# Kernel tuning notes

Hardware: AMD Instinct MI355X
Metric: run time of the kernel (lower is better)

Reference implementation:

```python
import jax, jax.numpy as jnp
import numpy as np
import math

N_NODES = 100000
N_EDGES = 3200000

_SQRT3 = math.sqrt(3.0)
_SQRT5 = math.sqrt(5.0)


def _spherical_harmonics_lmax2(v):
    """e3nn real spherical harmonics, lmax=2, normalize=True, normalization='component'.

    v: [E, 3] edge vectors (not necessarily unit).
    Returns [E, 9] = concat(Y0 [1], Y1 [3], Y2 [5]).
    """
    # normalize=True: evaluate SH on the unit vector
    u = v / jnp.linalg.norm(v, axis=1, keepdims=True)
    x, y, z = u[:, 0], u[:, 1], u[:, 2]
    # l=0 (component norm: *sqrt(1) = 1)
    sh0 = jnp.ones_like(x)
    # l=1 (component norm: *sqrt(3))
    sh1_0 = _SQRT3 * x
    sh1_1 = _SQRT3 * y
    sh1_2 = _SQRT3 * z
    # l=2 raw polynomials (norm-1 at unit vector), then *sqrt(5) for component norm
    x2, y2, z2 = x * x, y * y, z * z
    sh2_0 = _SQRT3 * x * z
    sh2_1 = _SQRT3 * x * y
    sh2_2 = y2 - 0.5 * (x2 + z2)
    sh2_3 = _SQRT3 * y * z
    sh2_4 = 0.5 * _SQRT3 * (z2 - x2)
    sh2 = _SQRT5 * jnp.stack([sh2_0, sh2_1, sh2_2, sh2_3, sh2_4], axis=-1)
    return jnp.concatenate(
        [sh0[:, None], jnp.stack([sh1_0, sh1_1, sh1_2], axis=-1), sh2], axis=-1
    )


def setup_inputs() -> dict:
    key = jax.random.key(0)
    k1, k2, k3 = jax.random.split(key, 3)
    pos = jax.random.normal(k1, (N_NODES, 3), dtype=jnp.float32)
    edge_index = jax.random.randint(k2, (2, N_EDGES), 0, N_NODES, dtype=jnp.int64)
    shift = jax.random.normal(k3, (N_EDGES, 3), dtype=jnp.float32)
    return {"pos": pos, "edge_index": edge_index, "shift": shift}


def reference(pos, edge_index, shift):
    # gather endpoints and form displacement vectors
    edge_vec = pos[edge_index[1]] - pos[edge_index[0]]  # [E, 3]
    edge_vec = edge_vec - shift
    edge_length = jnp.linalg.norm(edge_vec, axis=1)  # [E]
    edge_sh = _spherical_harmonics_lmax2(edge_vec)  # [E, 9]
    return (edge_vec, edge_length, edge_sh)
```

## Files before the change

kernel.cpp:

```cpp
#include <hip/hip_runtime.h>
#include <math.h>


#define SQRT3 1.7320508075688772f
#define SQRT5 2.2360679774997896f

__global__ __launch_bounds__(256) void sh_edge_kernel(
    const float* __restrict__ pos,
    const int*   __restrict__ edge_index,
    const float* __restrict__ shift,
    float* __restrict__ out_vec,
    float* __restrict__ out_len,
    float* __restrict__ out_sh,
    int n_edges)
{
    const int t  = blockIdx.x * blockDim.x + threadIdx.x;
    const int e0 = t * 4;
    if (e0 >= n_edges) return;

    float vx[4], vy[4], vz[4], len[4];
    float ux[4], uy[4], uz[4];

    if (e0 + 3 < n_edges) {
        const int4 src4 = *reinterpret_cast<const int4*>(edge_index + e0);
        const int4 dst4 = *reinterpret_cast<const int4*>(edge_index + n_edges + e0);
        const float4* sb = reinterpret_cast<const float4*>(shift + 3 * (size_t)e0);
        float4 s0 = sb[0], s1 = sb[1], s2 = sb[2];

        const int srcs[4] = {src4.x, src4.y, src4.z, src4.w};
        const int dsts[4] = {dst4.x, dst4.y, dst4.z, dst4.w};
        const float sx[4] = {s0.x, s0.w, s1.z, s2.y};
        const float sy[4] = {s0.y, s1.x, s1.w, s2.z};
        const float sz[4] = {s0.z, s1.y, s2.x, s2.w};

        #pragma unroll
        for (int i = 0; i < 4; ++i) {
            const float* ps = pos + 3 * (size_t)srcs[i];
            const float* pd = pos + 3 * (size_t)dsts[i];
            float x = pd[0] - ps[0] - sx[i];
            float y = pd[1] - ps[1] - sy[i];
            float z = pd[2] - ps[2] - sz[i];
            vx[i] = x; vy[i] = y; vz[i] = z;
            float sq = x * x + y * y + z * z;
            float r  = rsqrtf(sq);
            len[i]   = sq * r;
            ux[i] = x * r; uy[i] = y * r; uz[i] = z * r;
        }

        float4* ov = reinterpret_cast<float4*>(out_vec + 3 * (size_t)e0);
        ov[0] = make_float4(vx[0], vy[0], vz[0], vx[1]);
        ov[1] = make_float4(vy[1], vz[1], vx[2], vy[2]);
        ov[2] = make_float4(vz[2], vx[3], vy[3], vz[3]);

        *reinterpret_cast<float4*>(out_len + e0) =
            make_float4(len[0], len[1], len[2], len[3]);

        float shb[36];
        #pragma unroll
        for (int i = 0; i < 4; ++i) {
            float x = ux[i], y = uy[i], z = uz[i];
            float x2 = x * x, y2 = y * y, z2 = z * z;
            float* o = shb + 9 * i;
            o[0] = 1.0f;
            o[1] = SQRT3 * x;
            o[2] = SQRT3 * y;
            o[3] = SQRT3 * z;
            o[4] = SQRT5 * SQRT3 * x * z;
            o[5] = SQRT5 * SQRT3 * x * y;
            o[6] = SQRT5 * (y2 - 0.5f * (x2 + z2));
            o[7] = SQRT5 * SQRT3 * y * z;
            o[8] = SQRT5 * 0.5f * SQRT3 * (z2 - x2);
        }
        float4* os = reinterpret_cast<float4*>(out_sh + 9 * (size_t)e0);
        #pragma unroll
        for (int j = 0; j < 9; ++j) {
            os[j] = make_float4(shb[4 * j + 0], shb[4 * j + 1],
                                shb[4 * j + 2], shb[4 * j + 3]);
        }
    } else {
        for (int e = e0; e < n_edges; ++e) {
            int s = edge_index[e];
            int d = edge_index[n_edges + e];
            float x = pos[3 * (size_t)d + 0] - pos[3 * (size_t)s + 0] - shift[3 * (size_t)e + 0];
            float y = pos[3 * (size_t)d + 1] - pos[3 * (size_t)s + 1] - shift[3 * (size_t)e + 1];
            float z = pos[3 * (size_t)d + 2] - pos[3 * (size_t)s + 2] - shift[3 * (size_t)e + 2];
            out_vec[3 * (size_t)e + 0] = x;
            out_vec[3 * (size_t)e + 1] = y;
            out_vec[3 * (size_t)e + 2] = z;
            float sq = x * x + y * y + z * z;
            float r  = rsqrtf(sq);
            out_len[e] = sq * r;
            float nx = x * r, ny = y * r, nz = z * r;
            float x2 = nx * nx, y2 = ny * ny, z2 = nz * nz;
            float* o = out_sh + 9 * (size_t)e;
            o[0] = 1.0f;
            o[1] = SQRT3 * nx;
            o[2] = SQRT3 * ny;
            o[3] = SQRT3 * nz;
            o[4] = SQRT5 * SQRT3 * nx * nz;
            o[5] = SQRT5 * SQRT3 * nx * ny;
            o[6] = SQRT5 * (y2 - 0.5f * (x2 + z2));
            o[7] = SQRT5 * SQRT3 * ny * nz;
            o[8] = SQRT5 * 0.5f * SQRT3 * (z2 - x2);
        }
    }
}

extern "C" void kernel_launch(void* const* d_in, const int* in_sizes, int n_in,
                              void* d_out, int out_size, void* d_ws, size_t ws_size,
                              hipStream_t stream) {
    const float* pos        = (const float*)d_in[0];
    const int*   edge_index = (const int*)d_in[1];
    const float* shift      = (const float*)d_in[2];

    const int n_edges = in_sizes[2] / 3;

    float* out_vec = (float*)d_out;
    float* out_len = (float*)d_out + 3 * (size_t)n_edges;
    float* out_sh  = (float*)d_out + 4 * (size_t)n_edges;

    const int threads  = 256;
    const int n_thr    = (n_edges + 3) / 4;
    const int blocks   = (n_thr + threads - 1) / threads;

    sh_edge_kernel<<<blocks, threads, 0, stream>>>(
        pos, edge_index, shift, out_vec, out_len, out_sh, n_edges);
}
```

Baseline: 267.7 us.

## Pad positions to float4 and stage edge I/O through shared memory

```diff
diff --git a/kernel.cpp b/kernel.cpp
--- a/kernel.cpp
+++ b/kernel.cpp
@@ -5,104 +5,108 @@
 #define SQRT3 1.7320508075688772f
 #define SQRT5 2.2360679774997896f
 
+__global__ __launch_bounds__(256) void pack_pos4(
+    const float* __restrict__ pos, float4* __restrict__ pos4, int n)
+{
+    int i = blockIdx.x * blockDim.x + threadIdx.x;
+    if (i < n) {
+        pos4[i] = make_float4(pos[3 * (size_t)i + 0],
+                              pos[3 * (size_t)i + 1],
+                              pos[3 * (size_t)i + 2], 0.0f);
+    }
+}
+
 __global__ __launch_bounds__(256) void sh_edge_kernel(
-    const float* __restrict__ pos,
-    const int*   __restrict__ edge_index,
-    const float* __restrict__ shift,
+    const float4* __restrict__ pos4,
+    const float*  __restrict__ pos,
+    const int*    __restrict__ edge_index,
+    const float*  __restrict__ shift,
     float* __restrict__ out_vec,
     float* __restrict__ out_len,
     float* __restrict__ out_sh,
     int n_edges)
 {
-    const int t  = blockIdx.x * blockDim.x + threadIdx.x;
-    const int e0 = t * 4;
-    if (e0 >= n_edges) return;
+    __shared__ float s_shift[768];
+    __shared__ float s_vec[768];
+    __shared__ float s_len[256];
+    __shared__ float s_sh[2304];
 
-    float vx[4], vy[4], vz[4], len[4];
-    float ux[4], uy[4], uz[4];
+    const int tid  = threadIdx.x;
+    const int base = blockIdx.x * 256;
+    const int nblk = min(256, n_edges - base);
+    const bool full = (nblk == 256);
 
-    if (e0 + 3 < n_edges) {
-        const int4 src4 = *reinterpret_cast<const int4*>(edge_index + e0);
-        const int4 dst4 = *reinterpret_cast<const int4*>(edge_index + n_edges + e0);
-        const float4* sb = reinterpret_cast<const float4*>(shift + 3 * (size_t)e0);
-        float4 s0 = sb[0], s1 = sb[1], s2 = sb[2];
+    if (full) {
+        const float4* g = reinterpret_cast<const float4*>(shift + 3 * (size_t)base);
+        if (tid < 192) reinterpret_cast<float4*>(s_shift)[tid] = g[tid];
+    } else {
+        for (int i = tid; i < 3 * nblk; i += 256)
+            s_shift[i] = shift[3 * (size_t)base + i];
+    }
+    __syncthreads();
 
-        const int srcs[4] = {src4.x, src4.y, src4.z, src4.w};
-        const int dsts[4] = {dst4.x, dst4.y, dst4.z, dst4.w};
-        const float sx[4] = {s0.x, s0.w, s1.z, s2.y};
-        const float sy[4] = {s0.y, s1.x, s1.w, s2.z};
-        const float sz[4] = {s0.z, s1.y, s2.x, s2.w};
+    if (tid < nblk) {
+        const int e = base + tid;
+        const int s = edge_index[e];
+        const int d = edge_index[n_edges + e];
 
-        #pragma unroll
-        for (int i = 0; i < 4; ++i) {
-            const float* ps = pos + 3 * (size_t)srcs[i];
-            const float* pd = pos + 3 * (size_t)dsts[i];
-            float x = pd[0] - ps[0] - sx[i];
-            float y = pd[1] - ps[1] - sy[i];
-            float z = pd[2] - ps[2] - sz[i];
-            vx[i] = x; vy[i] = y; vz[i] = z;
-            float sq = x * x + y * y + z * z;
-            float r  = rsqrtf(sq);
-            len[i]   = sq * r;
-            ux[i] = x * r; uy[i] = y * r; uz[i] = z * r;
+        float psx, psy, psz, pdx, pdy, pdz;
+        if (pos4) {
+            float4 ps = pos4[s];
+            float4 pd = pos4[d];
+            psx = ps.x; psy = ps.y; psz = ps.z;
+            pdx = pd.x; pdy = pd.y; pdz = pd.z;
+        } else {
+            psx = pos[3 * (size_t)s + 0]; psy = pos[3 * (size_t)s + 1]; psz = pos[3 * (size_t)s + 2];
+            pdx = pos[3 * (size_t)d + 0]; pdy = pos[3 * (size_t)d + 1]; pdz = pos[3 * (size_t)d + 2];
         }
 
-        float4* ov = reinterpret_cast<float4*>(out_vec + 3 * (size_t)e0);
-        ov[0] = make_float4(vx[0], vy[0], vz[0], vx[1]);
-        ov[1] = make_float4(vy[1], vz[1], vx[2], vy[2]);
-        ov[2] = make_float4(vz[2], vx[3], vy[3], vz[3]);
+        float x = pdx - psx - s_shift[3 * tid + 0];
+        float y = pdy - psy - s_shift[3 * tid + 1];
+        float z = pdz - psz - s_shift[3 * tid + 2];
 
-        *reinterpret_cast<float4*>(out_len + e0) =
-            make_float4(len[0], len[1], len[2], len[3]);
+        s_vec[3 * tid + 0] = x;
+        s_vec[3 * tid + 1] = y;
+        s_vec[3 * tid + 2] = z;
 
-        float shb[36];
-        #pragma unroll
-        for (int i = 0; i < 4; ++i) {
-            float x = ux[i], y = uy[i], z = uz[i];
-            float x2 = x * x, y2 = y * y, z2 = z * z;
-            float* o = shb + 9 * i;
-            o[0] = 1.0f;
-            o[1] = SQRT3 * x;
-            o[2] = SQRT3 * y;
-            o[3] = SQRT3 * z;
-            o[4] = SQRT5 * SQRT3 * x * z;
-            o[5] = SQRT5 * SQRT3 * x * y;
-            o[6] = SQRT5 * (y2 - 0.5f * (x2 + z2));
-            o[7] = SQRT5 * SQRT3 * y * z;
-            o[8] = SQRT5 * 0.5f * SQRT3 * (z2 - x2);
-        }
-        float4* os = reinterpret_cast<float4*>(out_sh + 9 * (size_t)e0);
-        #pragma unroll
-        for (int j = 0; j < 9; ++j) {
-            os[j] = make_float4(shb[4 * j + 0], shb[4 * j + 1],
-                                shb[4 * j + 2], shb[4 * j + 3]);
-        }
+        float sq = x * x + y * y + z * z;
+        float r  = rsqrtf(sq);
+        s_len[tid] = sq * r;
+
+        float nx = x * r, ny = y * r, nz = z * r;
+        float x2 = nx * nx, y2 = ny * ny, z2 = nz * nz;
+
+        float* o = s_sh + 9 * tid;
+        o[0] = 1.0f;
+        o[1] = SQRT3 * nx;
+        o[2] = SQRT3 * ny;
+        o[3] = SQRT3 * nz;
+        o[4] = SQRT5 * SQRT3 * nx * nz;
+        o[5] = SQRT5 * SQRT3 * nx * ny;
+        o[6] = SQRT5 * (y2 - 0.5f * (x2 + z2));
+        o[7] = SQRT5 * SQRT3 * ny * nz;
+        o[8] = SQRT5 * 0.5f * SQRT3 * (z2 - x2);
+    }
+    __syncthreads();
+
+    if (full) {
+        float4* gv = reinterpret_cast<float4*>(out_vec + 3 * (size_t)base);
+        const float4* lv = reinterpret_cast<const float4*>(s_vec);
+        if (tid < 192) gv[tid] = lv[tid];
+
+        float4* gl = reinterpret_cast<float4*>(out_len + (size_t)base);
+        const float4* ll = reinterpret_cast<const float4*>(s_len);
+        if (tid < 64) gl[tid] = ll[tid];
+
+        float4* gs = reinterpret_cast<float4*>(out_sh + 9 * (size_t)base);
+        const float4* ls = reinterpret_cast<const float4*>(s_sh);
+        gs[tid]       = ls[tid];
+        gs[256 + tid] = ls[256 + tid];
+        if (tid < 64) gs[512 + tid] = ls[512 + tid];
     } else {
-        for (int e = e0; e < n_edges; ++e) {
-            int s = edge_index[e];
-            int d = edge_index[n_edges + e];
-            float x = pos[3 * (size_t)d + 0] - pos[3 * (size_t)s + 0] - shift[3 * (size_t)e + 0];
-            float y = pos[3 * (size_t)d + 1] - pos[3 * (size_t)s + 1] - shift[3 * (size_t)e + 1];
-            float z = pos[3 * (size_t)d + 2] - pos[3 * (size_t)s + 2] - shift[3 * (size_t)e + 2];
-            out_vec[3 * (size_t)e + 0] = x;
-            out_vec[3 * (size_t)e + 1] = y;
-            out_vec[3 * (size_t)e + 2] = z;
-            float sq = x * x + y * y + z * z;
-            float r  = rsqrtf(sq);
-            out_len[e] = sq * r;
-            float nx = x * r, ny = y * r, nz = z * r;
-            float x2 = nx * nx, y2 = ny * ny, z2 = nz * nz;
-            float* o = out_sh + 9 * (size_t)e;
-            o[0] = 1.0f;
-            o[1] = SQRT3 * nx;
-            o[2] = SQRT3 * ny;
-            o[3] = SQRT3 * nz;
-            o[4] = SQRT5 * SQRT3 * nx * nz;
-            o[5] = SQRT5 * SQRT3 * nx * ny;
-            o[6] = SQRT5 * (y2 - 0.5f * (x2 + z2));
-            o[7] = SQRT5 * SQRT3 * ny * nz;
-            o[8] = SQRT5 * 0.5f * SQRT3 * (z2 - x2);
-        }
+        for (int i = tid; i < 3 * nblk; i += 256) out_vec[3 * (size_t)base + i] = s_vec[i];
+        for (int i = tid; i < nblk;     i += 256) out_len[(size_t)base + i]     = s_len[i];
+        for (int i = tid; i < 9 * nblk; i += 256) out_sh[9 * (size_t)base + i]  = s_sh[i];
     }
 }
 
@@ -113,16 +117,21 @@
     const int*   edge_index = (const int*)d_in[1];
     const float* shift      = (const float*)d_in[2];
 
+    const int n_nodes = in_sizes[0] / 3;
     const int n_edges = in_sizes[2] / 3;
 
     float* out_vec = (float*)d_out;
     float* out_len = (float*)d_out + 3 * (size_t)n_edges;
     float* out_sh  = (float*)d_out + 4 * (size_t)n_edges;
 
-    const int threads  = 256;
-    const int n_thr    = (n_edges + 3) / 4;
-    const int blocks   = (n_thr + threads - 1) / threads;
+    float4* pos4 = nullptr;
+    if (ws_size >= (size_t)n_nodes * sizeof(float4)) {
+        pos4 = (float4*)d_ws;
+        int blocks = (n_nodes + 255) / 256;
+        pack_pos4<<<blocks, 256, 0, stream>>>(pos, pos4, n_nodes);
+    }
 
-    sh_edge_kernel<<<blocks, threads, 0, stream>>>(
-        pos, edge_index, shift, out_vec, out_len, out_sh, n_edges);
+    const int blocks = (n_edges + 255) / 256;
+    sh_edge_kernel<<<blocks, 256, 0, stream>>>(
+        pos4, pos, edge_index, shift, out_vec, out_len, out_sh, n_edges);
 }
```

After: 239.2 us. -10.6%, faster.
